# Kernel optimization log

Measured on AMD Instinct MI355X. Metric: run time of the kernel, lower is better.

## Reference

```python
import jax, jax.numpy as jnp
import numpy as np

VOCAB = 128
HID = 128
SEQ = 65536


def setup_inputs() -> dict:
    key = jax.random.key(0)
    ks = jax.random.split(key, 12)
    u = lambda k, shape, s: jax.random.uniform(k, shape, jnp.float32, -s, s)
    sA = 1.0 / np.sqrt(VOCAB)
    sH = 1.0 / np.sqrt(HID)
    return {
        "x": jax.random.normal(ks[0], (1, SEQ, VOCAB), jnp.float32),
        "hA": jnp.zeros((1, HID), jnp.float32),
        "cA": jnp.zeros((1, HID), jnp.float32),
        "hB": jnp.zeros((1, HID), jnp.float32),
        "cB": jnp.zeros((1, HID), jnp.float32),
        "WA1": u(ks[1], (4 * HID, VOCAB), sA), "bA1": u(ks[2], (4 * HID,), sA),
        "WA2": u(ks[3], (4 * HID, HID), sH), "bA2": u(ks[4], (4 * HID,), sH),
        "WB1": u(ks[5], (4 * HID, HID), sH), "bB1": u(ks[6], (4 * HID,), sH),
        "WB2": u(ks[7], (4 * HID, HID), sH), "bB2": u(ks[8], (4 * HID,), sH),
        # init_weights(): fc.weight ~ U(-1,1), fc.bias = 0
        "Wfc": jax.random.uniform(ks[9], (VOCAB, HID), jnp.float32, -1.0, 1.0),
        "bfc": jnp.zeros((VOCAB,), jnp.float32),
    }


def _lstm_cell(x_in, h, c, W1, b1, W2, b2):
    gates = x_in @ W1.T + b1 + h @ W2.T + b2  # [1, 4H]
    i, f, g, o = jnp.split(gates, 4, axis=-1)
    c = jax.nn.sigmoid(f) * c + jax.nn.sigmoid(i) * jnp.tanh(g)
    h = jax.nn.sigmoid(o) * jnp.tanh(c)
    return h, c


def reference(x, hA, cA, hB, cB, WA1, bA1, WA2, bA2, WB1, bB1, WB2, bB2, Wfc, bfc):
    # original takes x.unbind(0)[0] -> iterate over timesteps of batch element 0
    inputs = x[0][:, None, :]  # [S, 1, V]

    def step(carry, xt):
        hA, cA, hB, cB = carry
        hA, cA = _lstm_cell(xt, hA, cA, WA1, bA1, WA2, bA2)
        hB, cB = _lstm_cell(hA, hB, cB, WB1, bB1, WB2, bB2)
        return (hA, cA, hB, cB), hB

    (hA, cA, hB, cB), outs = jax.lax.scan(step, (hA, cA, hB, cB), inputs)
    # dropout is identity in eval; reshape [S,1,H] -> [S*1,H], then fc
    logits = outs.reshape(-1, HID) @ Wfc.T + bfc  # [S, VOCAB]
    return logits, hA, cA, hB, cB
```

## Files before the change

kernel.cpp:

```cpp
#include <hip/hip_runtime.h>

typedef unsigned short u16;
typedef unsigned int   u32;
typedef __bf16 bf16x8 __attribute__((ext_vector_type(8)));
typedef float  f32x4  __attribute__((ext_vector_type(4)));

#define T_SEQ 65536

__device__ __forceinline__ float bf2f(u16 v){ return __uint_as_float(((u32)v) << 16); }
__device__ __forceinline__ float bflo(u32 w){ return __uint_as_float(w << 16); }
__device__ __forceinline__ float bfhi(u32 w){ return __uint_as_float(w & 0xFFFF0000u); }
__device__ __forceinline__ u16 f2bf(float f){
  u32 u = __float_as_uint(f);
  u32 r = (u + 0x7FFFu + ((u >> 16) & 1u)) >> 16;
  return (u16)r;
}
__device__ __forceinline__ float sigm(float x){ return 1.0f / (1.0f + __expf(-x)); }
__device__ __forceinline__ float tanh_(float x){ return 1.0f - 2.0f / (1.0f + __expf(2.0f * x)); }

__device__ __forceinline__ float ldf(const void* p, size_t i, int f){
  return f ? ((const float*)p)[i] : bf2f(((const u16*)p)[i]);
}
__device__ __forceinline__ void stf(void* p, size_t i, float v, int f){
  if (f) ((float*)p)[i] = v; else ((u16*)p)[i] = f2bf(v);
}

__device__ __forceinline__ bf16x8 ldg_frag(const u16* p){
  uint4 v = *(const uint4*)p;
  return __builtin_bit_cast(bf16x8, v);
}
__device__ __forceinline__ bf16x8 load_frag_dyn(const void* p, int off, int f){
  if (!f) return ldg_frag((const u16*)p + off);
  union { u16 h[8]; bf16x8 v; } t;
  const float* q = (const float*)p + off;
#pragma unroll
  for (int j = 0; j < 8; ++j) t.h[j] = f2bf(q[j]);
  return t.v;
}
__device__ __forceinline__ bf16x8 lds_frag(const u16* p){
  uint4 v = *(const uint4*)p;
  return __builtin_bit_cast(bf16x8, v);
}

struct Ptrs { const void* p[15]; int n[15]; };

__global__ void k_detect(Ptrs ptrs, int* flags){
  const int i = threadIdx.x;
  if (i >= 15) return;
  const u32* w = (const u32*)ptrs.p[i];
  int words = ptrs.n[i] >> 1; if (words > 256) words = 256;
  int bad = 0, good = 0;
  for (int j = 0; j < words; ++j){
    u32 lo = w[j] & 0xFFFFu;
    if (lo == 0) continue;
    u32 e = (lo >> 7) & 0xFFu;
    if (e >= 96 && e <= 135) ++good; else ++bad;
  }
  flags[i] = (bad > good) ? 1 : 0;
}

__global__ __launch_bounds__(512) void k_gemm(const void* __restrict__ in, const void* __restrict__ W,
                                              const void* __restrict__ b1, const void* __restrict__ b2,
                                              const int* __restrict__ flags,
                                              int fiIn, int fiW, int fiB1, int fiB2,
                                              u16* __restrict__ out, int tbase){
  __shared__ __align__(16) float sx[32 * 128];
  const int fin = (fiIn < 0) ? 0 : flags[fiIn];
  const int fw = flags[fiW], f1 = flags[fiB1], f2 = flags[fiB2];
  const int tid = threadIdx.x;
  const int tl0 = blockIdx.x * 32;
  const int tg0 = tbase + tl0;
  for (int i = tid; i < 32 * 128; i += 512) sx[i] = ldf(in, (size_t)tg0 * 128 + i, fin);
  __syncthreads();
  const int r = tid;
  float bias = ldf(b1, r, f1) + ldf(b2, r, f2);
  float acc[32];
#pragma unroll
  for (int t = 0; t < 32; ++t) acc[t] = bias;
  if (!fw){
    const u32* wrow = (const u32*)W + r * 64;
    for (int c = 0; c < 32; ++c){
      uint2 wp = *(const uint2*)(wrow + 2 * c);
      float w0 = bflo(wp.x), w1 = bfhi(wp.x), w2 = bflo(wp.y), w3 = bfhi(wp.y);
#pragma unroll
      for (int t = 0; t < 32; ++t){
        const f32x4 xv = *(const f32x4*)&sx[t * 128 + 4 * c];
        acc[t] += w0 * xv.x + w1 * xv.y + w2 * xv.z + w3 * xv.w;
      }
    }
  } else {
    const float* wrow = (const float*)W + r * 128;
    for (int c = 0; c < 32; ++c){
      const f32x4 wv = *(const f32x4*)(wrow + 4 * c);
#pragma unroll
      for (int t = 0; t < 32; ++t){
        const f32x4 xv = *(const f32x4*)&sx[t * 128 + 4 * c];
        acc[t] += wv.x * xv.x + wv.y * xv.y + wv.z * xv.z + wv.w * xv.w;
      }
    }
  }
  for (int t = 0; t < 32; ++t) out[(size_t)(tl0 + t) * 512 + r] = f2bf(acc[t]);
}

__global__ __launch_bounds__(512, 2) void k_dual(
    const u16* __restrict__ preA, u16* __restrict__ preB,
    u16* __restrict__ hAws, u16* __restrict__ hb,
    const void* __restrict__ WA2, const void* __restrict__ WB1, const void* __restrict__ WB2,
    const void* __restrict__ hA0, const void* __restrict__ cA0,
    const void* __restrict__ hB0, const void* __restrict__ cB0,
    const void* __restrict__ bB1, const void* __restrict__ bB2,
    const int* __restrict__ flags, u32* __restrict__ flagA, u32* __restrict__ flagP,
    u16* __restrict__ stH, float* __restrict__ stC,
    void* __restrict__ outBase, int first, int last, int L)
{
  __shared__ __align__(16) u16   sPre[2][16 * 512];
  __shared__ __align__(16) u16   sHd[16 * 128];
  __shared__ __align__(16) float sG[512];
  __shared__ __align__(16) u16   sH[128];

  const int tid = threadIdx.x;
  const int w = tid >> 6, l = tid & 63, q = l >> 4, m = l & 15;
  const int fo = flags[0];
  const int role = blockIdx.x;
  const int G = L >> 4;

  if (role == 1){
    const int fW = flags[9], f1 = flags[10], f2 = flags[12];
    bf16x8 wf[4][4];
#pragma unroll
    for (int rt = 0; rt < 4; ++rt){
      const int row = (w * 4 + rt) * 16 + m;
#pragma unroll
      for (int kt = 0; kt < 4; ++kt)
        wf[rt][kt] = load_frag_dyn(WB1, row * 128 + kt * 32 + q * 8, fW);
    }
    float bias[4][4];
#pragma unroll
    for (int rt = 0; rt < 4; ++rt)
#pragma unroll
      for (int rg = 0; rg < 4; ++rg){
        const int r = (w * 4 + rt) * 16 + q * 4 + rg;
        bias[rt][rg] = ldf(bB1, r, f1) + ldf(bB2, r, f2);
      }
    for (int g = 0; g < G; ++g){
      if (tid == 0){
        while (atomicAdd(&flagA[g], 0u) == 0u) __builtin_amdgcn_s_sleep(8);
      }
      __syncthreads();
      const u16* hg = hAws + (size_t)g * 2048;
      f32x4 acc[4];
#pragma unroll
      for (int rt = 0; rt < 4; ++rt) acc[rt] = (f32x4){0.f, 0.f, 0.f, 0.f};
#pragma unroll
      for (int kt = 0; kt < 4; ++kt){
        bf16x8 bfrag = ldg_frag(hg + m * 128 + kt * 32 + q * 8);
#pragma unroll
        for (int rt = 0; rt < 4; ++rt)
          acc[rt] = __builtin_amdgcn_mfma_f32_16x16x32_bf16(wf[rt][kt], bfrag, acc[rt], 0, 0, 0);
      }
      const int tg = g * 16 + m;
#pragma unroll
      for (int rt = 0; rt < 4; ++rt){
        ushort4 o;
        o.x = f2bf(acc[rt].x + bias[rt][0]);
        o.y = f2bf(acc[rt].y + bias[rt][1]);
        o.z = f2bf(acc[rt].z + bias[rt][2]);
        o.w = f2bf(acc[rt].w + bias[rt][3]);
        *(ushort4*)(preB + (size_t)tg * 512 + (w * 4 + rt) * 16 + q * 4) = o;
      }
      __threadfence();
      __syncthreads();
      if (tid == 0) atomicExch(&flagP[g], 1u);
    }
    return;
  }

  const bool isA = (role == 0);
  const u16* pre = isA ? preA : preB;
  u16* hdump = isA ? hAws : hb;
  const void* Wm = isA ? WA2 : WB2;
  const void* h0 = isA ? hA0 : hB0;
  const void* c0 = isA ? cA0 : cB0;
  const int fW  = isA ? flags[7] : flags[11];
  const int fH0 = isA ? flags[1] : flags[3];
  const int fC0 = isA ? flags[2] : flags[4];
  const int sto = isA ? 0 : 128;

  bf16x8 wf[4][4];
#pragma unroll
  for (int rt = 0; rt < 4; ++rt){
    const int row = (w * 4 + rt) * 16 + m;
#pragma unroll
    for (int kt = 0; kt < 4; ++kt)
      wf[rt][kt] = load_frag_dyn(Wm, row * 128 + kt * 32 + q * 8, fW);
  }

  float c = 0.f;
  if (tid < 128){
    if (first){
      c = ldf(c0, tid, fC0);
      sH[tid] = f2bf(ldf(h0, tid, fH0));
    } else {
      c = stC[sto + tid];
      sH[tid] = stH[sto + tid];
    }
  }
  if (isA){
    const uint4* src = (const uint4*)pre;
    uint4* dst = (uint4*)&sPre[0][0];
    dst[tid]       = src[tid];
    dst[tid + 512] = src[tid + 512];
  }
  __syncthreads();

  for (int t = 0; t < L; ++t){
    const int slot = t & 15;
    const int buf  = isA ? ((t >> 4) & 1) : 0;

    uint4 st0, st1;
    bool doStage = false;
    int nc = 0;
    if (slot == 0){
      if (isA){
        if (t > 0 && tid < 256){
          const uint4* s = (const uint4*)sHd;
          ((uint4*)hdump)[(size_t)(t - 16) * 16 + tid] = s[tid];
          __threadfence();
        }
        nc = (t >> 4) + 1;
        if (nc < G){
          doStage = true;
          const uint4* src = (const uint4*)pre;
          st0 = src[(size_t)nc * 1024 + tid];
          st1 = src[(size_t)nc * 1024 + 512 + tid];
        }
      } else {
        const int g = t >> 4;
        if (tid == 0){
          while (atomicAdd(&flagP[g], 0u) == 0u) __builtin_amdgcn_s_sleep(8);
        }
        __syncthreads();
        const uint4* src = (const uint4*)(pre + (size_t)g * 8192);
        uint4* dst = (uint4*)&sPre[0][0];
        dst[tid]       = src[tid];
        dst[tid + 512] = src[tid + 512];
        if (t > 0 && tid < 256){
          const uint4* s = (const uint4*)sHd;
          ((uint4*)hdump)[(size_t)(t - 16) * 16 + tid] = s[tid];
        }
        __syncthreads();
      }
    }

    float pp0, pp1, pp2, pp3;
    if (tid < 128){
      const u16* pc = &sPre[buf][slot * 512];
      pp0 = bf2f(pc[tid]);
      pp1 = bf2f(pc[128 + tid]);
      pp2 = bf2f(pc[256 + tid]);
      pp3 = bf2f(pc[384 + tid]);
    }

    bf16x8 bh[4];
#pragma unroll
    for (int kt = 0; kt < 4; ++kt) bh[kt] = lds_frag(&sH[kt * 32 + q * 8]);
    f32x4 g[4];
#pragma unroll
    for (int rt = 0; rt < 4; ++rt) g[rt] = (f32x4){0.f, 0.f, 0.f, 0.f};
#pragma unroll
    for (int kt = 0; kt < 4; ++kt){
#pragma unroll
      for (int rt = 0; rt < 4; ++rt)
        g[rt] = __builtin_amdgcn_mfma_f32_16x16x32_bf16(wf[rt][kt], bh[kt], g[rt], 0, 0, 0);
    }
    if (m == 0){
#pragma unroll
      for (int rt = 0; rt < 4; ++rt)
        *(f32x4*)&sG[(w * 4 + rt) * 16 + q * 4] = g[rt];
    }
    if (doStage){
      uint4* dst = (uint4*)&sPre[nc & 1][0];
      dst[tid]       = st0;
      dst[tid + 512] = st1;
    }
    __syncthreads();

    if (isA && slot == 0 && t > 0 && tid == 448)
      atomicExch(&flagA[(t >> 4) - 1], 1u);

    if (tid < 128){
      float gi = sigm (pp0 + sG[tid]);
      float gf = sigm (pp1 + sG[128 + tid]);
      float gg = tanh_(pp2 + sG[256 + tid]);
      float go = sigm (pp3 + sG[384 + tid]);
      c = gf * c + gi * gg;
      u16 hq = f2bf(go * tanh_(c));
      sH[tid] = hq;
      sHd[slot * 128 + tid] = hq;
    }
    __syncthreads();
  }

  if (tid < 256){
    const uint4* s = (const uint4*)sHd;
    ((uint4*)hdump)[(size_t)(L - 16) * 16 + tid] = s[tid];
    __threadfence();
  }
  __syncthreads();
  if (isA && tid == 0) atomicExch(&flagA[G - 1], 1u);
  if (tid < 128){
    stC[sto + tid] = c;
    stH[sto + tid] = sH[tid];
    if (last){
      const size_t ob = (size_t)T_SEQ * 128;
      const size_t hOff = isA ? 0 : 256;
      const size_t cOff = isA ? 128 : 384;
      stf(outBase, ob + hOff + tid, bf2f(sH[tid]), fo);
      stf(outBase, ob + cOff + tid, c,             fo);
    }
  }
}

__global__ __launch_bounds__(256) void k_fc(const u16* __restrict__ hb,
                                            const void* __restrict__ Wfc, const void* __restrict__ bfc,
                                            const int* __restrict__ flags,
                                            void* __restrict__ out, int t0){
  __shared__ __align__(16) float sh[32 * 128];
  const int fw = flags[13], fb = flags[14], fo = flags[0];
  const int tid = threadIdx.x;
  const int tl0 = blockIdx.x * 32;
  for (int i = tid; i < 32 * 128; i += 256) sh[i] = bf2f(hb[(size_t)tl0 * 128 + i]);
  __syncthreads();
  const int v  = tid & 127;
  const int tt = tid >> 7;
  float bias = ldf(bfc, v, fb);
  float acc[16];
#pragma unroll
  for (int j = 0; j < 16; ++j) acc[j] = bias;
  if (!fw){
    const u32* wrow = (const u32*)Wfc + v * 64;
    for (int c = 0; c < 32; ++c){
      uint2 wp = *(const uint2*)(wrow + 2 * c);
      float w0 = bflo(wp.x), w1 = bfhi(wp.x), w2 = bflo(wp.y), w3 = bfhi(wp.y);
#pragma unroll
      for (int j = 0; j < 16; ++j){
        const f32x4 xv = *(const f32x4*)&sh[(tt + 2 * j) * 128 + 4 * c];
        acc[j] += w0 * xv.x + w1 * xv.y + w2 * xv.z + w3 * xv.w;
      }
    }
  } else {
    const float* wrow = (const float*)Wfc + v * 128;
    for (int c = 0; c < 32; ++c){
      const f32x4 wv = *(const f32x4*)(wrow + 4 * c);
#pragma unroll
      for (int j = 0; j < 16; ++j){
        const f32x4 xv = *(const f32x4*)&sh[(tt + 2 * j) * 128 + 4 * c];
        acc[j] += wv.x * xv.x + wv.y * xv.y + wv.z * xv.z + wv.w * xv.w;
      }
    }
  }
  for (int j = 0; j < 16; ++j)
    stf(out, (size_t)(t0 + tl0 + tt + 2 * j) * 128 + v, acc[j], fo);
}

extern "C" void kernel_launch(void* const* d_in, const int* in_sizes, int n_in,
                              void* d_out, int out_size, void* d_ws, size_t ws_size,
                              hipStream_t stream) {
  int CHUNK = 32;
  size_t dataOff = 4096;
  for (int c = T_SEQ; c >= 32; c >>= 1){
    size_t G = (size_t)c / 16;
    size_t dOff = (2048 + 8 * G + 4095) & ~(size_t)4095;
    size_t need = dOff + (size_t)c * 2560;
    if (need <= ws_size){ CHUNK = c; dataOff = dOff; break; }
  }
  const size_t G = (size_t)CHUNK / 16;
  float* stC    = (float*)d_ws;
  u16*   stH    = (u16*)((char*)d_ws + 1024);
  int*   dflags = (int*)((char*)d_ws + 1536);
  u32*   flagA  = (u32*)((char*)d_ws + 2048);
  u32*   flagP  = (u32*)((char*)d_ws + 2048 + 4 * G);
  u16*   preA   = (u16*)((char*)d_ws + dataOff);
  u16*   preB   = (u16*)((char*)d_ws + dataOff + (size_t)CHUNK * 1024);
  u16*   hAws   = (u16*)((char*)d_ws + dataOff + (size_t)CHUNK * 2048);
  u16*   hb     = (u16*)((char*)d_ws + dataOff + (size_t)CHUNK * 2048 + (size_t)CHUNK * 256);

  Ptrs ptrs;
  for (int i = 0; i < 15; ++i){ ptrs.p[i] = d_in[i]; ptrs.n[i] = in_sizes[i]; }
  k_detect<<<1, 64, 0, stream>>>(ptrs, dflags);

  const int nChunks = T_SEQ / CHUNK;
  for (int c = 0; c < nChunks; ++c){
    const int t0 = c * CHUNK;
    const int first = (c == 0), last = (c == nChunks - 1);
    hipMemsetAsync(flagA, 0, 8 * G, stream);
    k_gemm<<<CHUNK / 32, 512, 0, stream>>>(d_in[0], d_in[5], d_in[6], d_in[8], dflags,
                                           0, 5, 6, 8, preA, t0);
    k_dual<<<3, 512, 0, stream>>>(preA, preB, hAws, hb,
                                  d_in[7], d_in[9], d_in[11],
                                  d_in[1], d_in[2], d_in[3], d_in[4],
                                  d_in[10], d_in[12],
                                  dflags, flagA, flagP, stH, stC,
                                  d_out, first, last, CHUNK);
    k_fc  <<<CHUNK / 32, 256, 0, stream>>>(hb, d_in[13], d_in[14], dflags, d_out, t0);
  }
}
```

Before: 57.50 ms.

## Remap recurrent MFMA so gate math stays in registers with one barrier per step

The recurrent LSTM kernel reorders weight rows so each wave owns the i/f/g/o rows for the same 16 hidden units. It also swaps the MFMA operands, so each lane gets all four gate sums in its own registers. This removes the shared-memory gate buffer and one of the two barriers per timestep, and double-buffers the h vector. The B role now prefetches the next chunk of A-side activations one group ahead, instead of stalling at each chunk boundary. Hidden states go straight to global memory each step rather than being batched in shared memory, which means many small writes and redundant gate math in the lanes with q≠0.

```diff
diff --git a/kernel.cpp b/kernel.cpp
--- a/kernel.cpp
+++ b/kernel.cpp
@@ -40,6 +40,12 @@
 __device__ __forceinline__ bf16x8 lds_frag(const u16* p){
   uint4 v = *(const uint4*)p;
   return __builtin_bit_cast(bf16x8, v);
+}
+
+__device__ __forceinline__ void bar_sync(){
+  asm volatile("s_waitcnt lgkmcnt(0)" ::: "memory");
+  __builtin_amdgcn_s_barrier();
+  asm volatile("" ::: "memory");
 }
 
 struct Ptrs { const void* p[15]; int n[15]; };
@@ -113,10 +119,8 @@
     u16* __restrict__ stH, float* __restrict__ stC,
     void* __restrict__ outBase, int first, int last, int L)
 {
-  __shared__ __align__(16) u16   sPre[2][16 * 512];
-  __shared__ __align__(16) u16   sHd[16 * 128];
-  __shared__ __align__(16) float sG[512];
-  __shared__ __align__(16) u16   sH[128];
+  __shared__ __align__(16) u16 sPre[2][16 * 512];
+  __shared__ __align__(16) u16 sH[2][128];
 
   const int tid = threadIdx.x;
   const int w = tid >> 6, l = tid & 63, q = l >> 4, m = l & 15;
@@ -189,23 +193,29 @@
   bf16x8 wf[4][4];
 #pragma unroll
   for (int rt = 0; rt < 4; ++rt){
-    const int row = (w * 4 + rt) * 16 + m;
+    const int row = rt * 128 + w * 16 + m;
 #pragma unroll
     for (int kt = 0; kt < 4; ++kt)
       wf[rt][kt] = load_frag_dyn(Wm, row * 128 + kt * 32 + q * 8, fW);
   }
 
-  float c = 0.f;
-  if (tid < 128){
-    if (first){
-      c = ldf(c0, tid, fC0);
-      sH[tid] = f2bf(ldf(h0, tid, fH0));
-    } else {
-      c = stC[sto + tid];
-      sH[tid] = stH[sto + tid];
-    }
-  }
-  if (isA){
+  const int j = w * 16 + m;
+  float c;
+  if (first){
+    c = ldf(c0, j, fC0);
+    if (tid < 128) sH[0][tid] = f2bf(ldf(h0, tid, fH0));
+  } else {
+    c = stC[sto + j];
+    if (tid < 128) sH[0][tid] = stH[sto + tid];
+  }
+
+  if (!isA){
+    if (tid == 0){
+      while (atomicAdd(&flagP[0], 0u) == 0u) __builtin_amdgcn_s_sleep(8);
+    }
+    __syncthreads();
+  }
+  {
     const uint4* src = (const uint4*)pre;
     uint4* dst = (uint4*)&sPre[0][0];
     dst[tid]       = src[tid];
@@ -213,110 +223,96 @@
   }
   __syncthreads();
 
+  uint4 st0, st1;
+  int pend = 0, pbuf = 0;
+  u16 hq = 0;
+
   for (int t = 0; t < L; ++t){
     const int slot = t & 15;
-    const int buf  = isA ? ((t >> 4) & 1) : 0;
-
-    uint4 st0, st1;
-    bool doStage = false;
-    int nc = 0;
+    const int g = t >> 4;
+    const int buf = g & 1;
+    const int rb = t & 1;
+
     if (slot == 0){
       if (isA){
-        if (t > 0 && tid < 256){
-          const uint4* s = (const uint4*)sHd;
-          ((uint4*)hdump)[(size_t)(t - 16) * 16 + tid] = s[tid];
-          __threadfence();
-        }
-        nc = (t >> 4) + 1;
+        if (g > 0) __threadfence();
+        const int nc = g + 1;
         if (nc < G){
-          doStage = true;
           const uint4* src = (const uint4*)pre;
           st0 = src[(size_t)nc * 1024 + tid];
           st1 = src[(size_t)nc * 1024 + 512 + tid];
+          pend = 1; pbuf = nc & 1;
         }
+      }
+    } else if (slot == 1){
+      if (isA){
+        if (g > 0 && tid == 448) atomicExch(&flagA[g - 1], 1u);
       } else {
-        const int g = t >> 4;
-        if (tid == 0){
-          while (atomicAdd(&flagP[g], 0u) == 0u) __builtin_amdgcn_s_sleep(8);
+        const int nc = g + 1;
+        if (nc < G){
+          if (tid == 0){
+            while (atomicAdd(&flagP[nc], 0u) == 0u) __builtin_amdgcn_s_sleep(8);
+          }
+          bar_sync();
+          const uint4* src = (const uint4*)(pre + (size_t)nc * 8192);
+          st0 = src[tid];
+          st1 = src[tid + 512];
+          pend = 1; pbuf = nc & 1;
         }
-        __syncthreads();
-        const uint4* src = (const uint4*)(pre + (size_t)g * 8192);
-        uint4* dst = (uint4*)&sPre[0][0];
-        dst[tid]       = src[tid];
-        dst[tid + 512] = src[tid + 512];
-        if (t > 0 && tid < 256){
-          const uint4* s = (const uint4*)sHd;
-          ((uint4*)hdump)[(size_t)(t - 16) * 16 + tid] = s[tid];
-        }
-        __syncthreads();
-      }
-    }
-
-    float pp0, pp1, pp2, pp3;
-    if (tid < 128){
-      const u16* pc = &sPre[buf][slot * 512];
-      pp0 = bf2f(pc[tid]);
-      pp1 = bf2f(pc[128 + tid]);
-      pp2 = bf2f(pc[256 + tid]);
-      pp3 = bf2f(pc[384 + tid]);
-    }
+      }
+    } else if (slot == 2){
+      if (pend){
+        uint4* dst = (uint4*)&sPre[pbuf][0];
+        dst[tid]       = st0;
+        dst[tid + 512] = st1;
+        pend = 0;
+      }
+    }
+
+    const u16* pc = &sPre[buf][slot * 512 + j];
+    const float pp0 = bf2f(pc[0]);
+    const float pp1 = bf2f(pc[128]);
+    const float pp2 = bf2f(pc[256]);
+    const float pp3 = bf2f(pc[384]);
 
     bf16x8 bh[4];
 #pragma unroll
-    for (int kt = 0; kt < 4; ++kt) bh[kt] = lds_frag(&sH[kt * 32 + q * 8]);
-    f32x4 g[4];
-#pragma unroll
-    for (int rt = 0; rt < 4; ++rt) g[rt] = (f32x4){0.f, 0.f, 0.f, 0.f};
-#pragma unroll
-    for (int kt = 0; kt < 4; ++kt){
+    for (int kt = 0; kt < 4; ++kt) bh[kt] = lds_frag(&sH[rb][kt * 32 + q * 8]);
+
+    f32x4 acc[4];
+#pragma unroll
+    for (int rt = 0; rt < 4; ++rt) acc[rt] = (f32x4){0.f, 0.f, 0.f, 0.f};
+#pragma unroll
+    for (int kt = 0; kt < 4; ++kt)
 #pragma unroll
       for (int rt = 0; rt < 4; ++rt)
-        g[rt] = __builtin_amdgcn_mfma_f32_16x16x32_bf16(wf[rt][kt], bh[kt], g[rt], 0, 0, 0);
-    }
-    if (m == 0){
-#pragma unroll
-      for (int rt = 0; rt < 4; ++rt)
-        *(f32x4*)&sG[(w * 4 + rt) * 16 + q * 4] = g[rt];
-    }
-    if (doStage){
-      uint4* dst = (uint4*)&sPre[nc & 1][0];
-      dst[tid]       = st0;
-      dst[tid + 512] = st1;
-    }
-    __syncthreads();
-
-    if (isA && slot == 0 && t > 0 && tid == 448)
-      atomicExch(&flagA[(t >> 4) - 1], 1u);
-
-    if (tid < 128){
-      float gi = sigm (pp0 + sG[tid]);
-      float gf = sigm (pp1 + sG[128 + tid]);
-      float gg = tanh_(pp2 + sG[256 + tid]);
-      float go = sigm (pp3 + sG[384 + tid]);
-      c = gf * c + gi * gg;
-      u16 hq = f2bf(go * tanh_(c));
-      sH[tid] = hq;
-      sHd[slot * 128 + tid] = hq;
-    }
-    __syncthreads();
-  }
-
-  if (tid < 256){
-    const uint4* s = (const uint4*)sHd;
-    ((uint4*)hdump)[(size_t)(L - 16) * 16 + tid] = s[tid];
-    __threadfence();
-  }
+        acc[rt] = __builtin_amdgcn_mfma_f32_16x16x32_bf16(bh[kt], wf[rt][kt], acc[rt], 0, 0, 0);
+
+    const float gi = sigm (pp0 + acc[0].x);
+    const float gf = sigm (pp1 + acc[1].x);
+    const float gg = tanh_(pp2 + acc[2].x);
+    const float go = sigm (pp3 + acc[3].x);
+    c = gf * c + gi * gg;
+    hq = f2bf(go * tanh_(c));
+    if (q == 0){
+      sH[rb ^ 1][j] = hq;
+      hdump[(size_t)t * 128 + j] = hq;
+    }
+    bar_sync();
+  }
+
+  if (isA) __threadfence();
   __syncthreads();
   if (isA && tid == 0) atomicExch(&flagA[G - 1], 1u);
-  if (tid < 128){
-    stC[sto + tid] = c;
-    stH[sto + tid] = sH[tid];
+  if (q == 0){
+    stC[sto + j] = c;
+    stH[sto + j] = hq;
     if (last){
       const size_t ob = (size_t)T_SEQ * 128;
       const size_t hOff = isA ? 0 : 256;
       const size_t cOff = isA ? 128 : 384;
-      stf(outBase, ob + hOff + tid, bf2f(sH[tid]), fo);
-      stf(outBase, ob + cOff + tid, c,             fo);
+      stf(outBase, ob + hOff + j, bf2f(hq), fo);
+      stf(outBase, ob + cOff + j, c,        fo);
     }
   }
 }
```

After: 59.24 ms. 1.03x slower.
